# Kernel tuning notes

Hardware: AMD Instinct MI355X
Metric: run time of the kernel (lower is better)

The kernel has to match this reference:

```python
import jax, jax.numpy as jnp
import numpy as np

B, L = 1, 384
D_EDGE, D_BIAS, N_HEAD, D_HEAD = 128, 64, 4, 48
INF = 1000000.0
SCALE = 1.0 / np.sqrt(D_HEAD)
EPS = 1e-5


def _layernorm(x, g, b):
    mu = jnp.mean(x, axis=-1, keepdims=True)
    var = jnp.mean(jnp.square(x - mu), axis=-1, keepdims=True)
    return (x - mu) * jax.lax.rsqrt(var + EPS) * g + b


def _rope(x, pos):
    # x: [B, n, L, h, d], pos: [B, L] integer positions along the attended (i/j) axis
    half = x.shape[-1] // 2
    inv_freq = 1.0 / (10000.0 ** (jnp.arange(half, dtype=jnp.float32) / half))
    ang = pos.astype(jnp.float32)[..., None] * inv_freq          # [B, L, half]
    cos = jnp.cos(ang)[:, None, :, None, :]                       # [B,1,L,1,half]
    sin = jnp.sin(ang)[:, None, :, None, :]
    x1, x2 = jnp.split(x, 2, axis=-1)
    return jnp.concatenate([x1 * cos - x2 * sin, x1 * sin + x2 * cos], axis=-1)


def setup_inputs() -> dict:
    key = jax.random.key(0)
    ks = jax.random.split(key, 10)
    s = 0.02
    return {
        "edge": jax.random.normal(ks[0], (B, L, L, D_EDGE), jnp.float32),
        "bias": jax.random.normal(ks[1], (B, L, L, D_BIAS), jnp.float32),
        "edge_pos": jnp.arange(B * L, dtype=jnp.int32).reshape(B, L),
        "edge_mask": jnp.ones((B, L, L), jnp.float32),
        "ln_e_g": jnp.ones((D_EDGE,), jnp.float32),
        "ln_e_b": jnp.zeros((D_EDGE,), jnp.float32),
        "ln_b_g": jnp.ones((D_BIAS,), jnp.float32),
        "ln_b_b": jnp.zeros((D_BIAS,), jnp.float32),
        "Wq": jax.random.normal(ks[2], (D_EDGE, N_HEAD * D_HEAD), jnp.float32) * s,
        "Wk": jax.random.normal(ks[3], (D_EDGE, N_HEAD * D_HEAD), jnp.float32) * s,
        "Wv": jax.random.normal(ks[4], (D_EDGE, N_HEAD * D_HEAD), jnp.float32) * s,
        "Wb": jax.random.normal(ks[5], (D_BIAS, N_HEAD), jnp.float32) * s,
        "Wg": jax.random.normal(ks[6], (D_EDGE, N_HEAD * D_HEAD), jnp.float32) * s,
        "bg": jnp.zeros((N_HEAD * D_HEAD,), jnp.float32),
        "Wo": jax.random.normal(ks[7], (N_HEAD * D_HEAD, D_EDGE), jnp.float32) * s,
    }


def reference(edge, bias, edge_pos, edge_mask, ln_e_g, ln_e_b, ln_b_g, ln_b_b,
              Wq, Wk, Wv, Wb, Wg, bg, Wo):
    # is_row=True: swap the two residue axes of the pair representation
    e = jnp.transpose(edge, (0, 2, 1, 3))
    bi = jnp.transpose(bias, (0, 2, 1, 3))
    e = _layernorm(e, ln_e_g, ln_e_b)
    bi = _layernorm(bi, ln_b_g, ln_b_b)

    def proj(x, W):
        return (x @ W).reshape(B, L, L, N_HEAD, D_HEAD)

    q = proj(e, Wq)                      # [B, n, i, h, d]
    k = proj(e, Wk)
    v = proj(e, Wv)
    q = _rope(q, edge_pos)
    k = _rope(k, edge_pos)
    b_h = bi @ Wb                        # [B, i, j, h]
    gate = jax.nn.sigmoid(proj(e, Wg) + bg.reshape(1, 1, 1, N_HEAD, D_HEAD))

    q = q * SCALE
    k = k / L
    attn = jnp.einsum('bnihk,bnjhk->bijh', q, k) + b_h
    attn = jax.nn.softmax(attn, axis=-2)                 # softmax over j (dim -2)
    attn = attn + (INF * (edge_mask - 1.0))[..., None]    # post-softmax additive mask

    out = jnp.einsum('bijh,bnjhd->bnihd', attn, v)        # [B, n, i, h, d]
    out = gate * out
    out = out.reshape(B, L, L, N_HEAD * D_HEAD) @ Wo      # [B, n, i, d_edge]
    return jnp.transpose(out, (0, 2, 1, 3))               # undo row permute
```

## Files before the change

kernel.cpp:

```cpp
#include <hip/hip_runtime.h>
#include <hip/hip_bf16.h>


#define LQ 384
#define DE 128
#define DBI 64
#define NH 4
#define DH 48
#define NPOS (LQ*LQ)
#define KQK (LQ*DH)

typedef __attribute__((ext_vector_type(8))) short short8;
typedef __attribute__((ext_vector_type(4))) float f32x4;
typedef unsigned short u16;
typedef unsigned int u32;

__device__ __forceinline__ float b2f(u16 u) {
  union { u32 i; float f; } v; v.i = ((u32)u) << 16; return v.f;
}
__device__ __forceinline__ u16 f2b(float f) {
  __hip_bfloat16 h = __float2bfloat16(f);
  return __builtin_bit_cast(unsigned short, h);
}
__device__ __forceinline__ float wred_sum(float v) {
  #pragma unroll
  for (int o = 32; o; o >>= 1) v += __shfl_down(v, o);
  return __shfl(v, 0);
}

__device__ __forceinline__ void gemm_128x192(
    const u16* __restrict__ A, long lda, const u16* __restrict__ B, long ldb,
    int kTiles, u16* sA, u16* sB, f32x4 (&acc)[4][6])
{
  const int t = threadIdx.x;
  const int w = t >> 6, lane = t & 63, quad = lane >> 4, l16 = lane & 15;
  const int wr = w >> 1, wc = w & 1;
  for (int kt = 0; kt < kTiles; ++kt) {
    #pragma unroll
    for (int r = 0; r < 4; ++r) {
      int id = t + r * 256, row = id >> 3, c8 = (id & 7) * 8;
      *(uint4*)(sA + row * 72 + c8) = *(const uint4*)(A + (long)row * lda + kt * 64 + c8);
    }
    #pragma unroll
    for (int r = 0; r < 6; ++r) {
      int id = t + r * 256, row = id >> 3, c8 = (id & 7) * 8;
      *(uint4*)(sB + row * 72 + c8) = *(const uint4*)(B + (long)row * ldb + kt * 64 + c8);
    }
    __syncthreads();
    #pragma unroll
    for (int kk = 0; kk < 64; kk += 32) {
      short8 a[4], bf[6];
      #pragma unroll
      for (int rr = 0; rr < 4; ++rr)
        a[rr] = *(const short8*)(sA + (wr * 64 + rr * 16 + l16) * 72 + kk + quad * 8);
      #pragma unroll
      for (int f = 0; f < 6; ++f)
        bf[f] = *(const short8*)(sB + (wc * 96 + f * 16 + l16) * 72 + kk + quad * 8);
      #pragma unroll
      for (int rr = 0; rr < 4; ++rr)
        #pragma unroll
        for (int f = 0; f < 6; ++f)
          acc[rr][f] = __builtin_amdgcn_mfma_f32_16x16x32_bf16(a[rr], bf[f], acc[rr][f], 0, 0, 0);
    }
    __syncthreads();
  }
}

__global__ __launch_bounds__(256) void k_prep_w(
    const float* __restrict__ Wq, const float* __restrict__ Wk,
    const float* __restrict__ Wv, const float* __restrict__ Wg,
    const float* __restrict__ Wo, const int* __restrict__ epos,
    u16* __restrict__ WT, u16* __restrict__ WoT,
    float* __restrict__ cosT, float* __restrict__ sinT)
{
  int idx = blockIdx.x * 256 + threadIdx.x;
  if (idx < 768 * 128) {
    int col = idx >> 7, c = idx & 127;
    int which = col / 192, wi = col % 192;
    const float* W = (which == 0) ? Wq : (which == 1) ? Wk : (which == 2) ? Wv : Wg;
    WT[(long)col * 128 + c] = f2b(W[(long)c * 192 + wi]);
  }
  if (idx < 128 * 192) {
    int c = idx / 192, col = idx % 192;
    WoT[(long)c * 192 + col] = f2b(Wo[(long)col * 128 + c]);
  }
  if (idx < 384 * 24) {
    int i2 = idx / 24, dd = idx % 24;
    float ang = (float)epos[i2] * exp2f((float)dd * (-13.287712379549449f / 24.f));
    cosT[idx] = cosf(ang);
    sinT[idx] = sinf(ang);
  }
}

__global__ __launch_bounds__(256) void k_ln_e(
    const float* __restrict__ edge, const float* __restrict__ g,
    const float* __restrict__ b, u16* __restrict__ e_ln)
{
  int w = threadIdx.x >> 6, lane = threadIdx.x & 63;
  long p = (long)blockIdx.x * 4 + w;
  int n = (int)(p / LQ), i2 = (int)(p % LQ);
  const float* src = edge + ((long)i2 * LQ + n) * DE;
  float2 x = *(const float2*)(src + lane * 2);
  float mu = wred_sum(x.x + x.y) * (1.f / 128.f);
  float ms = wred_sum(x.x * x.x + x.y * x.y) * (1.f / 128.f);
  float r = rsqrtf(ms - mu * mu + 1e-5f);
  int c = lane * 2;
  u16 y0 = f2b((x.x - mu) * r * g[c] + b[c]);
  u16 y1 = f2b((x.y - mu) * r * g[c + 1] + b[c + 1]);
  *(u32*)(e_ln + p * DE + c) = (u32)y0 | ((u32)y1 << 16);
}

__global__ __launch_bounds__(256) void k_bias(
    const float* __restrict__ bias, const float* __restrict__ g,
    const float* __restrict__ b, const float* __restrict__ Wb,
    float* __restrict__ bh)
{
  int w = threadIdx.x >> 6, lane = threadIdx.x & 63;
  long q = (long)blockIdx.x * 4 + w;
  int i = (int)(q / LQ), j = (int)(q % LQ);
  float x = bias[((long)j * LQ + i) * DBI + lane];
  float mu = wred_sum(x) * (1.f / 64.f);
  float ms = wred_sum(x * x) * (1.f / 64.f);
  float r = rsqrtf(ms - mu * mu + 1e-5f);
  float y = (x - mu) * r * g[lane] + b[lane];
  #pragma unroll
  for (int h = 0; h < 4; ++h) {
    float v = y * Wb[lane * 4 + h];
    #pragma unroll
    for (int o = 32; o; o >>= 1) v += __shfl_down(v, o);
    if (lane == 0) bh[((long)h * LQ + i) * LQ + j] = v;
  }
}

__global__ __launch_bounds__(256) void k_proj(
    const u16* __restrict__ e_ln, const u16* __restrict__ WT,
    const float* __restrict__ cosT, const float* __restrict__ sinT,
    const float* __restrict__ bg,
    u16* __restrict__ q_buf, u16* __restrict__ k_buf,
    u16* __restrict__ vT, u16* __restrict__ gate)
{
  __shared__ __align__(16) u16 sA[128 * 136];
  __shared__ __align__(16) char sU[128 * 49 * 4];
  const int t = threadIdx.x;
  const int w = t >> 6, lane = t & 63, quad = lane >> 4, l16 = lane & 15;
  long mt = blockIdx.x;
  long pbase = mt * 128;
  int n = (int)(pbase / LQ), i2base = (int)(pbase % LQ);

  #pragma unroll
  for (int r = 0; r < 8; ++r) {
    int id = t + r * 256, row = id >> 4, c8 = (id & 15) * 8;
    *(uint4*)(sA + row * 136 + c8) = *(const uint4*)(e_ln + (pbase + row) * DE + c8);
  }
  __syncthreads();
  short8 a[2][4];
  #pragma unroll
  for (int rr = 0; rr < 2; ++rr)
    #pragma unroll
    for (int kki = 0; kki < 4; ++kki)
      a[rr][kki] = *(const short8*)(sA + (w * 32 + rr * 16 + l16) * 136 + kki * 32 + quad * 8);

  for (int cc = 0; cc < 16; ++cc) {
    int which = cc >> 2, h = cc & 3;
    u16* sB = (u16*)sU;
    #pragma unroll
    for (int r = 0; r < 3; ++r) {
      int id = t + r * 256, row = id >> 4, c8 = (id & 15) * 8;
      *(uint4*)(sB + row * 136 + c8) = *(const uint4*)(WT + ((long)cc * 48 + row) * DE + c8);
    }
    __syncthreads();
    f32x4 acc[2][3] = {};
    #pragma unroll
    for (int kki = 0; kki < 4; ++kki)
      #pragma unroll
      for (int f = 0; f < 3; ++f) {
        short8 bf = *(const short8*)(sB + (f * 16 + l16) * 136 + kki * 32 + quad * 8);
        acc[0][f] = __builtin_amdgcn_mfma_f32_16x16x32_bf16(a[0][kki], bf, acc[0][f], 0, 0, 0);
        acc[1][f] = __builtin_amdgcn_mfma_f32_16x16x32_bf16(a[1][kki], bf, acc[1][f], 0, 0, 0);
      }
    __syncthreads();
    float* sC = (float*)sU;
    #pragma unroll
    for (int rr = 0; rr < 2; ++rr)
      #pragma unroll
      for (int f = 0; f < 3; ++f)
        #pragma unroll
        for (int r = 0; r < 4; ++r)
          sC[(w * 32 + rr * 16 + quad * 4 + r) * 49 + f * 16 + l16] = acc[rr][f][r];
    __syncthreads();

    if (which < 2) {
      float scl = (which == 0) ? 0.14433756729740643f : (1.0f / 384.0f);
      u16* dst = (which == 0) ? q_buf : k_buf;
      #pragma unroll
      for (int it = 0; it < 3; ++it) {
        int id = t + it * 256;
        int row = id / 6, c8 = (id % 6) * 8;
        int i2 = i2base + row;
        const float* ct = cosT + i2 * 24;
        const float* st = sinT + i2 * 24;
        union { u16 s[8]; uint4 v; } o;
        #pragma unroll
        for (int u = 0; u < 8; ++u) {
          int d = c8 + u;
          int dd = (d < 24) ? d : d - 24;
          float x1 = sC[row * 49 + dd], x2 = sC[row * 49 + dd + 24];
          float y = (d < 24) ? (x1 * ct[dd] - x2 * st[dd]) : (x1 * st[dd] + x2 * ct[dd]);
          o.s[u] = f2b(y * scl);
        }
        *(uint4*)(dst + ((long)(h * LQ + i2) * LQ + n) * DH + c8) = o.v;
      }
    } else if (which == 2) {
      #pragma unroll
      for (int it = 0; it < 3; ++it) {
        int id = t + it * 256;
        int d = id >> 4, j8 = (id & 15) * 8;
        union { u16 s[8]; uint4 v; } o;
        #pragma unroll
        for (int u = 0; u < 8; ++u) o.s[u] = f2b(sC[(j8 + u) * 49 + d]);
        *(uint4*)(vT + ((long)h * KQK + n * DH + d) * LQ + i2base + j8) = o.v;
      }
    } else {
      #pragma unroll
      for (int it = 0; it < 3; ++it) {
        int id = t + it * 256;
        int row = id / 6, c8 = (id % 6) * 8;
        union { u16 s[8]; uint4 v; } o;
        #pragma unroll
        for (int u = 0; u < 8; ++u) {
          int d = c8 + u;
          float xx = sC[row * 49 + d] + bg[h * DH + d];
          o.s[u] = f2b(1.f / (1.f + __expf(-xx)));
        }
        *(uint4*)(gate + (pbase + row) * 192 + h * DH + c8) = o.v;
      }
    }
    __syncthreads();
  }
}

__global__ __launch_bounds__(256) void k_qk(
    const u16* __restrict__ q_buf, const u16* __restrict__ k_buf,
    float* __restrict__ partial)
{
  __shared__ __align__(16) u16 sA[128 * 72];
  __shared__ __align__(16) u16 sB[192 * 72];
  int nt = blockIdx.x & 1, s = blockIdx.x >> 1;
  int mt = blockIdx.y, h = blockIdx.z;
  f32x4 acc[4][6] = {};
  gemm_128x192(q_buf + ((long)h * LQ + mt * 128) * KQK + s * 768, KQK,
               k_buf + ((long)h * LQ + nt * 192) * KQK + s * 768, KQK,
               12, sA, sB, acc);
  const int t = threadIdx.x;
  const int w = t >> 6, lane = t & 63, quad = lane >> 4, l16 = lane & 15;
  const int wr = w >> 1, wc = w & 1;
  float* dst = partial + ((long)s * NH + h) * NPOS;
  #pragma unroll
  for (int rr = 0; rr < 4; ++rr)
    #pragma unroll
    for (int f = 0; f < 6; ++f)
      #pragma unroll
      for (int r = 0; r < 4; ++r) {
        int row = mt * 128 + wr * 64 + rr * 16 + quad * 4 + r;
        int col = nt * 192 + wc * 96 + f * 16 + l16;
        dst[(long)row * LQ + col] = acc[rr][f][r];
      }
}

__global__ __launch_bounds__(256) void k_softmax(
    const float* __restrict__ partial, const float* __restrict__ bh,
    const float* __restrict__ mask, u16* __restrict__ attn)
{
  int w = threadIdx.x >> 6, lane = threadIdx.x & 63;
  long row = (long)blockIdx.x * 4 + w;
  int i = (int)(row % LQ);
  float v[6];
  #pragma unroll
  for (int j0 = 0; j0 < 6; ++j0) v[j0] = bh[row * LQ + lane + j0 * 64];
  for (int s = 0; s < 24; ++s) {
    const float* p = partial + (long)s * NH * NPOS + row * LQ;
    #pragma unroll
    for (int j0 = 0; j0 < 6; ++j0) v[j0] += p[lane + j0 * 64];
  }
  float mx = -1e30f;
  #pragma unroll
  for (int j0 = 0; j0 < 6; ++j0) mx = fmaxf(mx, v[j0]);
  #pragma unroll
  for (int o = 32; o; o >>= 1) mx = fmaxf(mx, __shfl_down(mx, o));
  mx = __shfl(mx, 0);
  float sum = 0.f;
  #pragma unroll
  for (int j0 = 0; j0 < 6; ++j0) { v[j0] = __expf(v[j0] - mx); sum += v[j0]; }
  sum = wred_sum(sum);
  float inv = 1.f / sum;
  #pragma unroll
  for (int j0 = 0; j0 < 6; ++j0) {
    int j = lane + j0 * 64;
    float p = v[j0] * inv + 1.0e6f * (mask[(long)i * LQ + j] - 1.f);
    attn[row * LQ + j] = f2b(p);
  }
}

__global__ __launch_bounds__(256) void k_av(
    const u16* __restrict__ attn, const u16* __restrict__ vT,
    u16* __restrict__ out_buf)
{
  __shared__ __align__(16) u16 sA[128 * 72];
  __shared__ __align__(16) u16 sB[192 * 72];
  int nt = blockIdx.x, mt = blockIdx.y, h = blockIdx.z;
  f32x4 acc[4][6] = {};
  gemm_128x192(attn + ((long)h * LQ + mt * 128) * LQ, LQ,
               vT + ((long)h * KQK + nt * 192) * LQ, LQ,
               6, sA, sB, acc);
  const int t = threadIdx.x;
  const int w = t >> 6, lane = t & 63, quad = lane >> 4, l16 = lane & 15;
  const int wr = w >> 1, wc = w & 1;
  #pragma unroll
  for (int rr = 0; rr < 4; ++rr)
    #pragma unroll
    for (int f = 0; f < 6; ++f)
      #pragma unroll
      for (int r = 0; r < 4; ++r) {
        int i = mt * 128 + wr * 64 + rr * 16 + quad * 4 + r;
        int C = nt * 192 + wc * 96 + f * 16 + l16;
        int nn = C / 48, d = C - nn * 48;
        out_buf[((long)nn * LQ + i) * 192 + h * DH + d] = f2b(acc[rr][f][r]);
      }
}

__global__ __launch_bounds__(256) void k_out(
    const u16* __restrict__ out_buf, const u16* __restrict__ gate,
    const u16* __restrict__ WoT, float* __restrict__ outp)
{
  __shared__ __align__(16) u16 sA[128 * 72];
  __shared__ __align__(16) u16 sB[128 * 72];
  long mt = blockIdx.x;
  const int t = threadIdx.x;
  const int w = t >> 6, lane = t & 63, quad = lane >> 4, l16 = lane & 15;
  const int wr = w >> 1, wc = w & 1;
  f32x4 acc[4][4] = {};
  const u16* A1 = out_buf + mt * 128 * 192;
  const u16* A2 = gate + mt * 128 * 192;
  for (int kt = 0; kt < 3; ++kt) {
    #pragma unroll
    for (int r = 0; r < 4; ++r) {
      int id = t + r * 256, row = id >> 3, c8 = (id & 7) * 8;
      long off = (long)row * 192 + kt * 64 + c8;
      union { u16 s[8]; uint4 v; } ua, ub, ur;
      ua.v = *(const uint4*)(A1 + off);
      ub.v = *(const uint4*)(A2 + off);
      #pragma unroll
      for (int q2 = 0; q2 < 8; ++q2) ur.s[q2] = f2b(b2f(ua.s[q2]) * b2f(ub.s[q2]));
      *(uint4*)(sA + row * 72 + c8) = ur.v;
    }
    #pragma unroll
    for (int r = 0; r < 4; ++r) {
      int id = t + r * 256, row = id >> 3, c8 = (id & 7) * 8;
      *(uint4*)(sB + row * 72 + c8) = *(const uint4*)(WoT + (long)row * 192 + kt * 64 + c8);
    }
    __syncthreads();
    #pragma unroll
    for (int kk = 0; kk < 64; kk += 32) {
      short8 a[4], bf[4];
      #pragma unroll
      for (int rr = 0; rr < 4; ++rr)
        a[rr] = *(const short8*)(sA + (wr * 64 + rr * 16 + l16) * 72 + kk + quad * 8);
      #pragma unroll
      for (int f = 0; f < 4; ++f)
        bf[f] = *(const short8*)(sB + (wc * 64 + f * 16 + l16) * 72 + kk + quad * 8);
      #pragma unroll
      for (int rr = 0; rr < 4; ++rr)
        #pragma unroll
        for (int f = 0; f < 4; ++f)
          acc[rr][f] = __builtin_amdgcn_mfma_f32_16x16x32_bf16(a[rr], bf[f], acc[rr][f], 0, 0, 0);
    }
    __syncthreads();
  }
  long pbase = mt * 128;
  int n = (int)(pbase / LQ), ibase = (int)(pbase % LQ);
  #pragma unroll
  for (int rr = 0; rr < 4; ++rr)
    #pragma unroll
    for (int f = 0; f < 4; ++f)
      #pragma unroll
      for (int r = 0; r < 4; ++r) {
        int row = wr * 64 + rr * 16 + quad * 4 + r;
        int c = wc * 64 + f * 16 + l16;
        outp[((long)(ibase + row) * LQ + n) * DE + c] = acc[rr][f][r];
      }
}

extern "C" void kernel_launch(void* const* d_in, const int* in_sizes, int n_in,
                              void* d_out, int out_size, void* d_ws, size_t ws_size,
                              hipStream_t stream)
{
  const float* edge   = (const float*)d_in[0];
  const float* bias   = (const float*)d_in[1];
  const int*   epos   = (const int*)d_in[2];
  const float* mask   = (const float*)d_in[3];
  const float* ln_e_g = (const float*)d_in[4];
  const float* ln_e_b = (const float*)d_in[5];
  const float* ln_b_g = (const float*)d_in[6];
  const float* ln_b_b = (const float*)d_in[7];
  const float* Wq = (const float*)d_in[8];
  const float* Wk = (const float*)d_in[9];
  const float* Wv = (const float*)d_in[10];
  const float* Wb = (const float*)d_in[11];
  const float* Wg = (const float*)d_in[12];
  const float* bg = (const float*)d_in[13];
  const float* Wo = (const float*)d_in[14];
  float* outp = (float*)d_out;

  char* ws = (char*)d_ws;
  const size_t SZ = (size_t)NPOS * 192 * 2;
  u16* e_ln    = (u16*)ws;
  float* partial = (float*)ws;
  u16* out_buf = (u16*)ws;
  u16* q_buf   = (u16*)(ws + SZ);
  u16* k_buf   = (u16*)(ws + 2 * SZ);
  u16* vTb     = (u16*)(ws + 3 * SZ);
  u16* gateb   = (u16*)(ws + 4 * SZ);
  float* bh    = (float*)(ws + 5 * SZ);
  u16* attn    = (u16*)(ws + 5 * SZ + 2359296);
  u16* WT      = (u16*)(ws + 5 * SZ + 2359296 + 1179648);
  u16* WoT     = (u16*)(ws + 5 * SZ + 2359296 + 1179648 + 196608);
  float* cosT  = (float*)(ws + 5 * SZ + 2359296 + 1179648 + 196608 + 49152);
  float* sinT  = cosT + 384 * 24;

  k_prep_w<<<dim3(384), dim3(256), 0, stream>>>(Wq, Wk, Wv, Wg, Wo, epos, WT, WoT, cosT, sinT);
  k_bias<<<dim3(36864), dim3(256), 0, stream>>>(bias, ln_b_g, ln_b_b, Wb, bh);
  k_ln_e<<<dim3(36864), dim3(256), 0, stream>>>(edge, ln_e_g, ln_e_b, e_ln);
  k_proj<<<dim3(1152), dim3(256), 0, stream>>>(e_ln, WT, cosT, sinT, bg,
                                               q_buf, k_buf, vTb, gateb);
  k_qk<<<dim3(48, 3, 4), dim3(256), 0, stream>>>(q_buf, k_buf, partial);
  k_softmax<<<dim3(384), dim3(256), 0, stream>>>(partial, bh, mask, attn);
  k_av<<<dim3(96, 3, 4), dim3(256), 0, stream>>>(attn, vTb, out_buf);
  k_out<<<dim3(1152), dim3(256), 0, stream>>>(out_buf, gateb, WoT, outp);
}
```

Measured before the change: 641.7 us.

## Relayout q/k/out/gate buffers for coalesced writes and restructure QK, AV, output stores

```diff
diff --git a/kernel.cpp b/kernel.cpp
--- a/kernel.cpp
+++ b/kernel.cpp
@@ -136,11 +136,12 @@
     const u16* __restrict__ e_ln, const u16* __restrict__ WT,
     const float* __restrict__ cosT, const float* __restrict__ sinT,
     const float* __restrict__ bg,
-    u16* __restrict__ q_buf, u16* __restrict__ k_buf,
-    u16* __restrict__ vT, u16* __restrict__ gate)
+    u16* __restrict__ q48, u16* __restrict__ k48,
+    u16* __restrict__ vT, u16* __restrict__ gate3)
 {
   __shared__ __align__(16) u16 sA[128 * 136];
-  __shared__ __align__(16) char sU[128 * 49 * 4];
+  __shared__ __align__(16) u16 sB[48 * 136];
+  __shared__ __align__(16) float sC[128 * 49];
   const int t = threadIdx.x;
   const int w = t >> 6, lane = t & 63, quad = lane >> 4, l16 = lane & 15;
   long mt = blockIdx.x;
@@ -162,7 +163,6 @@
 
   for (int cc = 0; cc < 16; ++cc) {
     int which = cc >> 2, h = cc & 3;
-    u16* sB = (u16*)sU;
     #pragma unroll
     for (int r = 0; r < 3; ++r) {
       int id = t + r * 256, row = id >> 4, c8 = (id & 15) * 8;
@@ -178,8 +178,6 @@
         acc[0][f] = __builtin_amdgcn_mfma_f32_16x16x32_bf16(a[0][kki], bf, acc[0][f], 0, 0, 0);
         acc[1][f] = __builtin_amdgcn_mfma_f32_16x16x32_bf16(a[1][kki], bf, acc[1][f], 0, 0, 0);
       }
-    __syncthreads();
-    float* sC = (float*)sU;
     #pragma unroll
     for (int rr = 0; rr < 2; ++rr)
       #pragma unroll
@@ -191,7 +189,7 @@
 
     if (which < 2) {
       float scl = (which == 0) ? 0.14433756729740643f : (1.0f / 384.0f);
-      u16* dst = (which == 0) ? q_buf : k_buf;
+      u16* base = ((which == 0) ? q48 : k48) + ((long)(h * LQ + n) * LQ + i2base) * DH;
       #pragma unroll
       for (int it = 0; it < 3; ++it) {
         int id = t + it * 256;
@@ -208,7 +206,7 @@
           float y = (d < 24) ? (x1 * ct[dd] - x2 * st[dd]) : (x1 * st[dd] + x2 * ct[dd]);
           o.s[u] = f2b(y * scl);
         }
-        *(uint4*)(dst + ((long)(h * LQ + i2) * LQ + n) * DH + c8) = o.v;
+        *(uint4*)(base + (long)row * DH + c8) = o.v;
       }
     } else if (which == 2) {
       #pragma unroll
@@ -232,28 +230,61 @@
           float xx = sC[row * 49 + d] + bg[h * DH + d];
           o.s[u] = f2b(1.f / (1.f + __expf(-xx)));
         }
-        *(uint4*)(gate + (pbase + row) * 192 + h * DH + c8) = o.v;
-      }
-    }
-    __syncthreads();
+        *(uint4*)(gate3 + ((long)h * NPOS + pbase + row) * DH + c8) = o.v;
+      }
+    }
   }
 }
 
 __global__ __launch_bounds__(256) void k_qk(
-    const u16* __restrict__ q_buf, const u16* __restrict__ k_buf,
+    const u16* __restrict__ q48, const u16* __restrict__ k48,
     float* __restrict__ partial)
 {
-  __shared__ __align__(16) u16 sA[128 * 72];
-  __shared__ __align__(16) u16 sB[192 * 72];
+  __shared__ __align__(16) u16 sA[128 * 104];
+  __shared__ __align__(16) u16 sB[192 * 104];
   int nt = blockIdx.x & 1, s = blockIdx.x >> 1;
   int mt = blockIdx.y, h = blockIdx.z;
-  f32x4 acc[4][6] = {};
-  gemm_128x192(q_buf + ((long)h * LQ + mt * 128) * KQK + s * 768, KQK,
-               k_buf + ((long)h * LQ + nt * 192) * KQK + s * 768, KQK,
-               12, sA, sB, acc);
   const int t = threadIdx.x;
   const int w = t >> 6, lane = t & 63, quad = lane >> 4, l16 = lane & 15;
   const int wr = w >> 1, wc = w & 1;
+  f32x4 acc[4][6] = {};
+  for (int kt = 0; kt < 12; ++kt) {
+    int n0 = s * 24 + kt * 2;
+    #pragma unroll
+    for (int r = 0; r < 6; ++r) {
+      int p = r / 3;
+      int rem = t + (r - p * 3) * 256;
+      int row = rem / 6, c8 = (rem % 6) * 8;
+      *(uint4*)(sA + row * 104 + p * 48 + c8) =
+        *(const uint4*)(q48 + (((long)h * LQ + n0 + p) * LQ + mt * 128 + row) * DH + c8);
+    }
+    #pragma unroll
+    for (int r = 0; r < 9; ++r) {
+      int id = t + r * 256;
+      int p = (id >= 1152) ? 1 : 0;
+      int rem = id - p * 1152;
+      int row = rem / 6, c8 = (rem % 6) * 8;
+      *(uint4*)(sB + row * 104 + p * 48 + c8) =
+        *(const uint4*)(k48 + (((long)h * LQ + n0 + p) * LQ + nt * 192 + row) * DH + c8);
+    }
+    __syncthreads();
+    #pragma unroll
+    for (int kk = 0; kk < 96; kk += 32) {
+      short8 a[4], bf[6];
+      #pragma unroll
+      for (int rr = 0; rr < 4; ++rr)
+        a[rr] = *(const short8*)(sA + (wr * 64 + rr * 16 + l16) * 104 + kk + quad * 8);
+      #pragma unroll
+      for (int f = 0; f < 6; ++f)
+        bf[f] = *(const short8*)(sB + (wc * 96 + f * 16 + l16) * 104 + kk + quad * 8);
+      #pragma unroll
+      for (int rr = 0; rr < 4; ++rr)
+        #pragma unroll
+        for (int f = 0; f < 6; ++f)
+          acc[rr][f] = __builtin_amdgcn_mfma_f32_16x16x32_bf16(a[rr], bf[f], acc[rr][f], 0, 0, 0);
+    }
+    __syncthreads();
+  }
   float* dst = partial + ((long)s * NH + h) * NPOS;
   #pragma unroll
   for (int rr = 0; rr < 4; ++rr)
@@ -277,7 +308,7 @@
   float v[6];
   #pragma unroll
   for (int j0 = 0; j0 < 6; ++j0) v[j0] = bh[row * LQ + lane + j0 * 64];
-  for (int s = 0; s < 24; ++s) {
+  for (int s = 0; s < 16; ++s) {
     const float* p = partial + (long)s * NH * NPOS + row * LQ;
     #pragma unroll
     for (int j0 = 0; j0 < 6; ++j0) v[j0] += p[lane + j0 * 64];
@@ -303,71 +334,90 @@
 
 __global__ __launch_bounds__(256) void k_av(
     const u16* __restrict__ attn, const u16* __restrict__ vT,
-    u16* __restrict__ out_buf)
+    u16* __restrict__ out3)
 {
   __shared__ __align__(16) u16 sA[128 * 72];
   __shared__ __align__(16) u16 sB[192 * 72];
-  int nt = blockIdx.x, mt = blockIdx.y, h = blockIdx.z;
-  f32x4 acc[4][6] = {};
-  gemm_128x192(attn + ((long)h * LQ + mt * 128) * LQ, LQ,
-               vT + ((long)h * KQK + nt * 192) * LQ, LQ,
-               6, sA, sB, acc);
+  int nt = blockIdx.x, h = blockIdx.y;
   const int t = threadIdx.x;
   const int w = t >> 6, lane = t & 63, quad = lane >> 4, l16 = lane & 15;
   const int wr = w >> 1, wc = w & 1;
-  #pragma unroll
-  for (int rr = 0; rr < 4; ++rr)
-    #pragma unroll
-    for (int f = 0; f < 6; ++f)
-      #pragma unroll
-      for (int r = 0; r < 4; ++r) {
-        int i = mt * 128 + wr * 64 + rr * 16 + quad * 4 + r;
-        int C = nt * 192 + wc * 96 + f * 16 + l16;
-        int nn = C / 48, d = C - nn * 48;
-        out_buf[((long)nn * LQ + i) * 192 + h * DH + d] = f2b(acc[rr][f][r]);
-      }
+  for (int mt = 0; mt < 3; ++mt) {
+    f32x4 acc[4][6] = {};
+    gemm_128x192(attn + ((long)h * LQ + mt * 128) * LQ, LQ,
+                 vT + ((long)h * KQK + nt * 192) * LQ, LQ,
+                 6, sA, sB, acc);
+    u16* sCb = sB;
+    #pragma unroll
+    for (int ch = 0; ch < 2; ++ch) {
+      if (wc == ch) {
+        #pragma unroll
+        for (int rr = 0; rr < 4; ++rr)
+          #pragma unroll
+          for (int f = 0; f < 6; ++f)
+            #pragma unroll
+            for (int r = 0; r < 4; ++r)
+              sCb[(wr * 64 + rr * 16 + quad * 4 + r) * 104 + f * 16 + l16] = f2b(acc[rr][f][r]);
+      }
+      __syncthreads();
+      #pragma unroll
+      for (int r2 = 0; r2 < 6; ++r2) {
+        int id = t + r2 * 256;
+        int row = id / 12, u = id % 12;
+        int nnl = u / 6, c8 = (u % 6) * 8;
+        int nval = nt * 4 + ch * 2 + nnl;
+        *(uint4*)(out3 + ((long)h * NPOS + (long)nval * LQ + mt * 128 + row) * DH + c8) =
+          *(const uint4*)(sCb + row * 104 + nnl * 48 + c8);
+      }
+      __syncthreads();
+    }
+  }
 }
 
 __global__ __launch_bounds__(256) void k_out(
-    const u16* __restrict__ out_buf, const u16* __restrict__ gate,
+    const u16* __restrict__ out3, const u16* __restrict__ gate3,
     const u16* __restrict__ WoT, float* __restrict__ outp)
 {
-  __shared__ __align__(16) u16 sA[128 * 72];
-  __shared__ __align__(16) u16 sB[128 * 72];
+  __shared__ __align__(16) u16 sA[128 * 104];
+  __shared__ __align__(16) u16 sB[128 * 104];
   long mt = blockIdx.x;
+  long pbase = mt * 128;
   const int t = threadIdx.x;
   const int w = t >> 6, lane = t & 63, quad = lane >> 4, l16 = lane & 15;
   const int wr = w >> 1, wc = w & 1;
   f32x4 acc[4][4] = {};
-  const u16* A1 = out_buf + mt * 128 * 192;
-  const u16* A2 = gate + mt * 128 * 192;
-  for (int kt = 0; kt < 3; ++kt) {
-    #pragma unroll
-    for (int r = 0; r < 4; ++r) {
-      int id = t + r * 256, row = id >> 3, c8 = (id & 7) * 8;
-      long off = (long)row * 192 + kt * 64 + c8;
+  for (int kt = 0; kt < 2; ++kt) {
+    #pragma unroll
+    for (int r = 0; r < 6; ++r) {
+      int p = r / 3;
+      int rem = t + (r - p * 3) * 256;
+      int row = rem / 6, c8 = (rem % 6) * 8;
+      long off = ((long)(kt * 2 + p) * NPOS + pbase + row) * DH + c8;
       union { u16 s[8]; uint4 v; } ua, ub, ur;
-      ua.v = *(const uint4*)(A1 + off);
-      ub.v = *(const uint4*)(A2 + off);
+      ua.v = *(const uint4*)(out3 + off);
+      ub.v = *(const uint4*)(gate3 + off);
       #pragma unroll
       for (int q2 = 0; q2 < 8; ++q2) ur.s[q2] = f2b(b2f(ua.s[q2]) * b2f(ub.s[q2]));
-      *(uint4*)(sA + row * 72 + c8) = ur.v;
-    }
-    #pragma unroll
-    for (int r = 0; r < 4; ++r) {
-      int id = t + r * 256, row = id >> 3, c8 = (id & 7) * 8;
-      *(uint4*)(sB + row * 72 + c8) = *(const uint4*)(WoT + (long)row * 192 + kt * 64 + c8);
-    }
-    __syncthreads();
-    #pragma unroll
-    for (int kk = 0; kk < 64; kk += 32) {
+      *(uint4*)(sA + row * 104 + p * 48 + c8) = ur.v;
+    }
+    #pragma unroll
+    for (int r = 0; r < 6; ++r) {
+      int p = r / 3;
+      int rem = t + (r - p * 3) * 256;
+      int row = rem / 6, c8 = (rem % 6) * 8;
+      *(uint4*)(sB + row * 104 + p * 48 + c8) =
+        *(const uint4*)(WoT + (long)row * 192 + kt * 96 + p * 48 + c8);
+    }
+    __syncthreads();
+    #pragma unroll
+    for (int kk = 0; kk < 96; kk += 32) {
       short8 a[4], bf[4];
       #pragma unroll
       for (int rr = 0; rr < 4; ++rr)
-        a[rr] = *(const short8*)(sA + (wr * 64 + rr * 16 + l16) * 72 + kk + quad * 8);
+        a[rr] = *(const short8*)(sA + (wr * 64 + rr * 16 + l16) * 104 + kk + quad * 8);
       #pragma unroll
       for (int f = 0; f < 4; ++f)
-        bf[f] = *(const short8*)(sB + (wc * 64 + f * 16 + l16) * 72 + kk + quad * 8);
+        bf[f] = *(const short8*)(sB + (wc * 64 + f * 16 + l16) * 104 + kk + quad * 8);
       #pragma unroll
       for (int rr = 0; rr < 4; ++rr)
         #pragma unroll
@@ -376,18 +426,31 @@
     }
     __syncthreads();
   }
-  long pbase = mt * 128;
   int n = (int)(pbase / LQ), ibase = (int)(pbase % LQ);
-  #pragma unroll
-  for (int rr = 0; rr < 4; ++rr)
-    #pragma unroll
-    for (int f = 0; f < 4; ++f)
-      #pragma unroll
-      for (int r = 0; r < 4; ++r) {
-        int row = wr * 64 + rr * 16 + quad * 4 + r;
-        int c = wc * 64 + f * 16 + l16;
-        outp[((long)(ibase + row) * LQ + n) * DE + c] = acc[rr][f][r];
-      }
+  float* sAf = (float*)sA;
+  #pragma unroll
+  for (int pass = 0; pass < 4; ++pass) {
+    if (wr == (pass >> 1)) {
+      #pragma unroll
+      for (int rr2 = 0; rr2 < 2; ++rr2) {
+        int rr = (pass & 1) * 2 + rr2;
+        #pragma unroll
+        for (int f = 0; f < 4; ++f)
+          #pragma unroll
+          for (int r = 0; r < 4; ++r)
+            sAf[(rr2 * 16 + quad * 4 + r) * 132 + wc * 64 + f * 16 + l16] = acc[rr][f][r];
+      }
+    }
+    __syncthreads();
+    #pragma unroll
+    for (int r2 = 0; r2 < 4; ++r2) {
+      int id = t + r2 * 256;
+      int row32 = id >> 5, c4 = id & 31;
+      float4 v = *(const float4*)(sAf + row32 * 132 + c4 * 4);
+      *(float4*)(outp + ((long)(ibase + pass * 32 + row32) * LQ + n) * DE + c4 * 4) = v;
+    }
+    __syncthreads();
+  }
 }
 
 extern "C" void kernel_launch(void* const* d_in, const int* in_sizes, int n_in,
@@ -413,27 +476,27 @@
 
   char* ws = (char*)d_ws;
   const size_t SZ = (size_t)NPOS * 192 * 2;
-  u16* e_ln    = (u16*)ws;
+  u16* e_ln      = (u16*)ws;
   float* partial = (float*)ws;
-  u16* out_buf = (u16*)ws;
-  u16* q_buf   = (u16*)(ws + SZ);
-  u16* k_buf   = (u16*)(ws + 2 * SZ);
-  u16* vTb     = (u16*)(ws + 3 * SZ);
-  u16* gateb   = (u16*)(ws + 4 * SZ);
-  float* bh    = (float*)(ws + 5 * SZ);
-  u16* attn    = (u16*)(ws + 5 * SZ + 2359296);
-  u16* WT      = (u16*)(ws + 5 * SZ + 2359296 + 1179648);
-  u16* WoT     = (u16*)(ws + 5 * SZ + 2359296 + 1179648 + 196608);
-  float* cosT  = (float*)(ws + 5 * SZ + 2359296 + 1179648 + 196608 + 49152);
-  float* sinT  = cosT + 384 * 24;
+  u16* out3      = (u16*)ws;
+  u16* q48   = (u16*)(ws + SZ);
+  u16* k48   = (u16*)(ws + 2 * SZ);
+  u16* vTb   = (u16*)(ws + 3 * SZ);
+  u16* gate3 = (u16*)(ws + 4 * SZ);
+  float* bh  = (float*)(ws + 5 * SZ);
+  u16* attn  = (u16*)(ws + 5 * SZ + 2359296);
+  u16* WT    = (u16*)(ws + 5 * SZ + 2359296 + 1179648);
+  u16* WoT   = (u16*)(ws + 5 * SZ + 2359296 + 1179648 + 196608);
+  float* cosT = (float*)(ws + 5 * SZ + 2359296 + 1179648 + 196608 + 49152);
+  float* sinT = cosT + 384 * 24;
 
   k_prep_w<<<dim3(384), dim3(256), 0, stream>>>(Wq, Wk, Wv, Wg, Wo, epos, WT, WoT, cosT, sinT);
   k_bias<<<dim3(36864), dim3(256), 0, stream>>>(bias, ln_b_g, ln_b_b, Wb, bh);
   k_ln_e<<<dim3(36864), dim3(256), 0, stream>>>(edge, ln_e_g, ln_e_b, e_ln);
   k_proj<<<dim3(1152), dim3(256), 0, stream>>>(e_ln, WT, cosT, sinT, bg,
-                                               q_buf, k_buf, vTb, gateb);
-  k_qk<<<dim3(48, 3, 4), dim3(256), 0, stream>>>(q_buf, k_buf, partial);
+                                               q48, k48, vTb, gate3);
+  k_qk<<<dim3(32, 3, 4), dim3(256), 0, stream>>>(q48, k48, partial);
   k_softmax<<<dim3(384), dim3(256), 0, stream>>>(partial, bh, mask, attn);
-  k_av<<<dim3(96, 3, 4), dim3(256), 0, stream>>>(attn, vTb, out_buf);
-  k_out<<<dim3(1152), dim3(256), 0, stream>>>(out_buf, gateb, WoT, outp);
-}
+  k_av<<<dim3(96, 4), dim3(256), 0, stream>>>(attn, vTb, out3);
+  k_out<<<dim3(1152), dim3(256), 0, stream>>>(out3, gate3, WoT, outp);
+}
```

Result: no change. 642.6 us (+0.1%).
